# Optimization experiments

Hardware: AMD Instinct MI355X
Metric: run time of the kernel (lower is better)

## Reference

```python
import jax, jax.numpy as jnp
import numpy as np

H, W, HEADS, DIM_HEAD, SLICE = 256, 256, 8, 64, 64
SCALE = DIM_HEAD ** -0.5


def _conv(x_nhwc, w_hwio, b):
    y = jax.lax.conv_general_dilated(
        x_nhwc, w_hwio, window_strides=(1, 1), padding='SAME',
        dimension_numbers=('NHWC', 'HWIO', 'NHWC'))
    return y + b


def setup_inputs() -> dict:
    key = jax.random.key(0)
    ks = jax.random.split(key, 13)
    B, N, C, inner = 2, H * W, 128, HEADS * DIM_HEAD
    s = lambda k, shp, sc: jax.random.normal(k, shp, jnp.float32) * sc
    return {
        'x': s(ks[0], (B, N, C), 1.0),
        'Wfx': s(ks[1], (3, 3, C, inner), 0.05),
        'bfx': s(ks[2], (inner,), 0.02),
        'Wx': s(ks[3], (3, 3, C, inner), 0.05),
        'bx': s(ks[4], (inner,), 0.02),
        'Wslice': s(ks[5], (SLICE, DIM_HEAD), 0.1),
        'bslice': s(ks[6], (SLICE,), 0.02),
        'temperature': jnp.ones((1, HEADS, 1, 1), jnp.float32) * 0.5,
        'Wq': s(ks[7], (DIM_HEAD, DIM_HEAD), 0.1),
        'Wk': s(ks[8], (DIM_HEAD, DIM_HEAD), 0.1),
        'Wv': s(ks[9], (DIM_HEAD, DIM_HEAD), 0.1),
        'Wout': s(ks[10], (C, inner), 0.05),
        'bout': s(ks[11], (C,), 0.02),
    }


def reference(x, Wfx, bfx, Wx, bx, Wslice, bslice, temperature, Wq, Wk, Wv, Wout, bout):
    B, N, C = x.shape
    xg = x.reshape(B, H, W, C)                       # NHWC grid
    # conv QKV-style projections -> [B, heads, N, dim_head]
    def to_heads(y):
        return y.reshape(B, N, HEADS, DIM_HEAD).transpose(0, 2, 1, 3)
    fx_mid = to_heads(_conv(xg, Wfx, bfx))           # [B,h,N,d]
    x_mid = to_heads(_conv(xg, Wx, bx))              # [B,h,N,d]
    # slice assignment weights: softmax over slices with clamped temperature
    temp = jnp.clip(temperature, 0.1, 5.0)           # [1,h,1,1]
    logits = (jnp.einsum('bhnd,gd->bhng', x_mid, Wslice) + bslice) / temp
    slice_weights = jax.nn.softmax(logits, axis=-1)  # [B,h,N,G]
    slice_norm = slice_weights.sum(axis=2)           # [B,h,G]
    slice_token = jnp.einsum('bhnc,bhng->bhgc', fx_mid, slice_weights)
    slice_token = slice_token / (slice_norm + 1e-5)[..., None]  # [B,h,G,d]
    # small attention over slice tokens
    q = jnp.einsum('bhgd,ed->bhge', slice_token, Wq)
    k = jnp.einsum('bhgd,ed->bhge', slice_token, Wk)
    v = jnp.einsum('bhgd,ed->bhge', slice_token, Wv)
    attn = jax.nn.softmax(jnp.einsum('bhge,bhfe->bhgf', q, k) * SCALE, axis=-1)
    out_slice = jnp.einsum('bhgf,bhfe->bhge', attn, v)           # [B,h,G,d]
    # scatter back to tokens
    out_x = jnp.einsum('bhgc,bhng->bhnc', out_slice, slice_weights)
    out_x = out_x.transpose(0, 2, 1, 3).reshape(B, N, HEADS * DIM_HEAD)
    return jnp.einsum('bni,oi->bno', out_x, Wout) + bout
```

## Files before the change

kernel.cpp:

```cpp
#include <hip/hip_runtime.h>


typedef _Float16 f16;
typedef _Float16 f16x8 __attribute__((ext_vector_type(8)));
typedef _Float16 f16x4 __attribute__((ext_vector_type(4)));
typedef float    f32x4 __attribute__((ext_vector_type(4)));

static const size_t OFF_PADX = 0;
static const size_t OFF_WCAT = 17040384;
static const size_t OFF_ST   = 19399680;
static const size_t OFF_NORM = 19530752;
static const size_t OFF_OS   = 19532800;
static const size_t OFF_PT   = 19663872;
static const size_t OFF_XMID = 19794944;
static const size_t OFF_FXT  = 86903808;

__device__ __forceinline__ void ldsdma16(f16* lds, const f16* g) {
  __builtin_amdgcn_global_load_lds((__attribute__((address_space(1))) void*)g,
                                   (__attribute__((address_space(3))) void*)lds,
                                   16, 0, 0);
}

__global__ __launch_bounds__(256) void pad_kernel(const float* __restrict__ xb,
                                                  f16* __restrict__ padx) {
  int idx = blockIdx.x * 256 + threadIdx.x;
  if (idx >= 258 * 258 * 16) return;
  int c8 = (idx & 15) * 8;
  int r  = idx >> 4;
  int jp = r % 258;
  int ip = r / 258;
  f16x8 v;
  if (ip == 0 || ip == 257 || jp == 0 || jp == 257) {
#pragma unroll
    for (int j = 0; j < 8; ++j) v[j] = (f16)0.0f;
  } else {
    const float* src = xb + ((size_t)(ip - 1) * 256 + (jp - 1)) * 128 + c8;
#pragma unroll
    for (int j = 0; j < 8; ++j) v[j] = (f16)src[j];
  }
  *(f16x8*)(padx + (size_t)r * 128 + c8) = v;
}

__global__ __launch_bounds__(256) void prepw_kernel(const float* __restrict__ Wfx,
                                                    const float* __restrict__ Wx,
                                                    f16* __restrict__ wcat) {
  int idx = blockIdx.x * 256 + threadIdx.x;
  if (idx >= 9 * 1024 * 128) return;
  int ci = idx & 127;
  int t  = idx >> 7;
  int co = t & 1023;
  int tap = t >> 10;
  float v = (co < 512) ? Wfx[(size_t)(tap * 128 + ci) * 512 + co]
                       : Wx[(size_t)(tap * 128 + ci) * 512 + (co - 512)];
  wcat[idx] = (f16)v;
}

__global__ __launch_bounds__(256, 2) void conv_kernel(const f16* __restrict__ padx,
                                                      const f16* __restrict__ wcat,
                                                      const float* __restrict__ bfx,
                                                      const float* __restrict__ bx,
                                                      f16* __restrict__ xmid,
                                                      f16* __restrict__ fxT) {
  __shared__ f16 smem[33024];
  f16* As0 = smem;
  f16* As1 = smem + 8320;
  f16* Bs0 = smem + 16640;
  f16* Bs1 = smem + 24832;
  int tid = threadIdx.x;
  int wg = (blockIdx.x & 7) * 512 + (blockIdx.x >> 3);
  int nt = wg & 7;
  int mt = wg >> 3;
  int i  = mt >> 1;
  int j0 = (mt & 1) * 128;
  int n0 = nt * 128;
  int lane = tid & 63, wave = tid >> 6;
  int ln15 = lane & 15, quad = lane >> 4;
  int wm = wave & 1, wn = wave >> 1;

  f32x4 acc[4][4] = {};

  auto stageA = [&](int di, int kc, f16* dst) {
#pragma unroll
    for (int ph = 0; ph < 5; ++ph) {
      int s = ph * 256 + tid;
      if (ph < 4 || s < 1040) {
        int rr = s >> 3;
        int qq = ((s & 7) ^ (rr & 7)) * 8;
        ldsdma16(&dst[(ph * 256 + wave * 64) * 8],
                 padx + ((size_t)(i + di) * 258 + j0 + rr) * 128 + kc + qq);
      }
    }
  };
  auto stageB = [&](int tap, int kc, f16* dst) {
#pragma unroll
    for (int ph = 0; ph < 4; ++ph) {
      int s = ph * 256 + tid;
      int rr = s >> 3;
      int qq = ((s & 7) ^ (rr & 7)) * 8;
      ldsdma16(&dst[(ph * 256 + wave * 64) * 8],
               wcat + ((size_t)(tap * 1024 + n0 + rr)) * 128 + kc + qq);
    }
  };
  auto computePhase = [&](int dj, const f16* A, const f16* B) {
#pragma unroll
    for (int ks = 0; ks < 2; ++ks) {
      int q = ks * 4 + quad;
      f16x8 af[4], bfr[4];
#pragma unroll
      for (int xx = 0; xx < 4; ++xx) {
        int t  = dj + wm * 64 + xx * 16 + ln15;
        int rb = wn * 64 + xx * 16 + ln15;
        af[xx]  = *(const f16x8*)(&A[t * 64 + ((q ^ (t & 7)) * 8)]);
        bfr[xx] = *(const f16x8*)(&B[rb * 64 + ((q ^ (rb & 7)) * 8)]);
      }
      __builtin_amdgcn_s_setprio(1);
#pragma unroll
      for (int mf = 0; mf < 4; ++mf)
#pragma unroll
        for (int nf = 0; nf < 4; ++nf)
          acc[mf][nf] = __builtin_amdgcn_mfma_f32_16x16x32_f16(af[mf], bfr[nf],
                                                               acc[mf][nf], 0, 0, 0);
      __builtin_amdgcn_s_setprio(0);
    }
  };

  stageA(0, 0, As0);
  stageB(0, 0, Bs0);
  __syncthreads();

#pragma unroll
  for (int p = 0; p < 18; ++p) {
    int dj   = p % 3;
    int dikc = p / 3;
    if (p + 1 < 18) {
      int np = p + 1;
      int ndj = np % 3, ndikc = np / 3;
      int ndi = ndikc >> 1, nkc = (ndikc & 1) * 64;
      stageB(ndi * 3 + ndj, nkc, (np & 1) ? Bs1 : Bs0);
      if (ndj == 0) stageA(ndi, nkc, (ndikc & 1) ? As1 : As0);
    }
    computePhase(dj, (dikc & 1) ? As1 : As0, (p & 1) ? Bs1 : Bs0);
    __syncthreads();
  }

  size_t token0 = (size_t)i * 256 + j0;
  if (nt < 4) {
    f16* tile = smem;
#pragma unroll
    for (int nf = 0; nf < 4; ++nf) {
      int colLoc = wn * 64 + nf * 16 + ln15;
      float bias = bfx[n0 + colLoc];
#pragma unroll
      for (int mf = 0; mf < 4; ++mf) {
        int tokBase = wm * 64 + mf * 16 + quad * 4;
        f16x4 pk;
#pragma unroll
        for (int v = 0; v < 4; ++v) pk[v] = (f16)(acc[mf][nf][v] + bias);
        *(f16x4*)(&tile[colLoc * 136 + tokBase]) = pk;
      }
    }
    __syncthreads();
#pragma unroll
    for (int it2 = 0; it2 < 8; ++it2) {
      int s = it2 * 256 + tid;
      int c = s >> 4, t8 = s & 15;
      f16x8 vv = *(const f16x8*)(&tile[c * 136 + t8 * 8]);
      *(f16x8*)(fxT + (size_t)(n0 + c) * 65536 + token0 + t8 * 8) = vv;
    }
  } else {
#pragma unroll
    for (int nf = 0; nf < 4; ++nf) {
      int col = n0 + wn * 64 + nf * 16 + ln15;
      float bias = bx[col - 512];
#pragma unroll
      for (int mf = 0; mf < 4; ++mf) {
        int rbase = wm * 64 + mf * 16 + quad * 4;
#pragma unroll
        for (int v = 0; v < 4; ++v)
          xmid[(size_t)(token0 + rbase + v) * 512 + (col - 512)] =
              (f16)(acc[mf][nf][v] + bias);
      }
    }
  }
}

#define WS_S 72
#define WT_S 264
__global__ __launch_bounds__(256, 2) void slice_kernel(f16* __restrict__ xmid,
                                                       const f16* __restrict__ fxT,
                                                       const float* __restrict__ Wslice,
                                                       const float* __restrict__ bslice,
                                                       const float* __restrict__ temperature,
                                                       float* __restrict__ ST,
                                                       float* __restrict__ snorm) {
  __shared__ f16 Ws[64 * WS_S];
  __shared__ f16 Wt[64 * WT_S];
  __shared__ float red[64 * 65];
  __shared__ float redn[64];
  int tid = threadIdx.x;
  int h = blockIdx.x >> 6;
  int chunk = blockIdx.x & 63;
  int tok0 = chunk * 1024;
  int lane = tid & 63, wave = tid >> 6;
  int ln15 = lane & 15, quad = lane >> 4;

  for (int s = tid; s < 4096; s += 256)
    Ws[(s >> 6) * WS_S + (s & 63)] = (f16)Wslice[s];
  if (tid < 64) redn[tid] = 0.f;
  float tc = temperature[h];
  tc = fminf(fmaxf(tc, 0.1f), 5.0f);
  float invt = 1.0f / tc;
  float bsv[4];
#pragma unroll
  for (int nf = 0; nf < 4; ++nf) bsv[nf] = bslice[nf * 16 + ln15];
  __syncthreads();

  f32x4 acc2[4][4] = {};
  float naccv[4] = {};

  for (int it = 0; it < 4; ++it) {
    int tsub = it * 256 + wave * 64;
    f32x4 accA[4][4] = {};
#pragma unroll
    for (int kq = 0; kq < 2; ++kq) {
      f16x8 bf[4];
#pragma unroll
      for (int nf = 0; nf < 4; ++nf)
        bf[nf] = *(const f16x8*)(&Ws[(nf * 16 + ln15) * WS_S + kq * 32 + quad * 8]);
#pragma unroll
      for (int mf = 0; mf < 4; ++mf) {
        f16x8 af = *(const f16x8*)(xmid + (size_t)(tok0 + tsub + mf * 16 + ln15) * 512 +
                                   h * 64 + kq * 32 + quad * 8);
#pragma unroll
        for (int nf = 0; nf < 4; ++nf)
          accA[mf][nf] = __builtin_amdgcn_mfma_f32_16x16x32_f16(af, bf[nf], accA[mf][nf],
                                                                0, 0, 0);
      }
    }
#pragma unroll
    for (int mf = 0; mf < 4; ++mf) {
#pragma unroll
      for (int v = 0; v < 4; ++v) {
        float l[4];
#pragma unroll
        for (int nf = 0; nf < 4; ++nf) l[nf] = (accA[mf][nf][v] + bsv[nf]) * invt;
        float lm = fmaxf(fmaxf(l[0], l[1]), fmaxf(l[2], l[3]));
#pragma unroll
        for (int off = 1; off < 16; off <<= 1) lm = fmaxf(lm, __shfl_xor(lm, off, 64));
        float e[4], ssum = 0.f;
#pragma unroll
        for (int nf = 0; nf < 4; ++nf) { e[nf] = __expf(l[nf] - lm); ssum += e[nf]; }
#pragma unroll
        for (int off = 1; off < 16; off <<= 1) ssum += __shfl_xor(ssum, off, 64);
        float winv = 1.0f / ssum;
        int t_loc = tsub + mf * 16 + quad * 4 + v;
        int t_str = wave * 64 + mf * 16 + quad * 4 + v;
        f16* wrow = xmid + (size_t)(tok0 + t_loc) * 512 + h * 64;
#pragma unroll
        for (int nf = 0; nf < 4; ++nf) {
          float w = e[nf] * winv;
          naccv[nf] += w;
          f16 wh = (f16)w;
          wrow[nf * 16 + ln15] = wh;
          Wt[(nf * 16 + ln15) * WT_S + t_str] = wh;
        }
      }
    }
#pragma unroll
    for (int kq = 0; kq < 2; ++kq) {
      int kof = wave * 64 + kq * 32 + quad * 8;
      f16x8 bfB[4];
#pragma unroll
      for (int nf = 0; nf < 4; ++nf)
        bfB[nf] = *(const f16x8*)(fxT + (size_t)(h * 64 + nf * 16 + ln15) * 65536 +
                                  tok0 + it * 256 + kof);
#pragma unroll
      for (int mf = 0; mf < 4; ++mf) {
        f16x8 afB = *(const f16x8*)(&Wt[(mf * 16 + ln15) * WT_S + kof]);
#pragma unroll
        for (int nf = 0; nf < 4; ++nf)
          acc2[mf][nf] = __builtin_amdgcn_mfma_f32_16x16x32_f16(afB, bfB[nf],
                                                                acc2[mf][nf], 0, 0, 0);
      }
    }
  }

#pragma unroll
  for (int nf = 0; nf < 4; ++nf) atomicAdd(&redn[nf * 16 + ln15], naccv[nf]);

  for (int s = 0; s < 4; ++s) {
    if (wave == s) {
#pragma unroll
      for (int mf = 0; mf < 4; ++mf)
#pragma unroll
        for (int nf = 0; nf < 4; ++nf)
#pragma unroll
          for (int v = 0; v < 4; ++v) {
            int g = mf * 16 + quad * 4 + v;
            int d = nf * 16 + ln15;
            if (s == 0) red[g * 65 + d] = acc2[mf][nf][v];
            else        red[g * 65 + d] += acc2[mf][nf][v];
          }
    }
    __syncthreads();
  }
  float* stp = ST + (size_t)h * 4096;
  for (int s2 = tid; s2 < 4096; s2 += 256)
    atomicAdd(&stp[s2], red[(s2 >> 6) * 65 + (s2 & 63)]);
  if (tid < 64) atomicAdd(&snorm[h * 64 + tid], redn[tid]);
}

__global__ __launch_bounds__(256) void attn_pt_kernel(const float* __restrict__ ST,
                                                      const float* __restrict__ snorm,
                                                      const float* __restrict__ Wq,
                                                      const float* __restrict__ Wk,
                                                      const float* __restrict__ Wv,
                                                      const float* __restrict__ Wout,
                                                      f16* __restrict__ PT) {
  int h = blockIdx.x;
  __shared__ float tok[64 * 65];
  __shared__ float qs[64 * 65];
  __shared__ float ksm[64 * 65];
  __shared__ f16 vsm[64 * 65];
  int tid = threadIdx.x;
  const float* stp = ST + (size_t)h * 4096;
  const float* snp = snorm + (size_t)h * 64;
  for (int s = tid; s < 4096; s += 256) {
    int g = s >> 6, d = s & 63;
    tok[g * 65 + d] = stp[s] / (snp[g] + 1e-5f);
  }
  __syncthreads();
  int g = tid >> 2, p16 = (tid & 3) * 16;
  for (int e0 = 0; e0 < 16; ++e0) {
    int e = p16 + e0;
    const float* wq = Wq + e * 64;
    const float* wk = Wk + e * 64;
    const float* wv = Wv + e * 64;
    float aq = 0, ak = 0, av = 0;
#pragma unroll 8
    for (int d = 0; d < 64; ++d) {
      float tv = tok[g * 65 + d];
      aq += tv * wq[d];
      ak += tv * wk[d];
      av += tv * wv[d];
    }
    qs[g * 65 + e] = aq;
    ksm[g * 65 + e] = ak;
    vsm[g * 65 + e] = (f16)av;
  }
  __syncthreads();
  float* sc = tok;
  for (int f0 = 0; f0 < 16; ++f0) {
    int f = p16 + f0;
    float s = 0;
#pragma unroll 8
    for (int e = 0; e < 64; ++e) s += qs[g * 65 + e] * ksm[f * 65 + e];
    sc[g * 65 + f] = s * 0.125f;
  }
  __syncthreads();
  if (tid < 64) {
    float m = -1e30f;
    for (int f = 0; f < 64; ++f) m = fmaxf(m, sc[tid * 65 + f]);
    float ssum = 0;
    for (int f = 0; f < 64; ++f) {
      float e = __expf(sc[tid * 65 + f] - m);
      sc[tid * 65 + f] = e;
      ssum += e;
    }
    float inv = 1.0f / ssum;
    for (int f = 0; f < 64; ++f) sc[tid * 65 + f] *= inv;
  }
  __syncthreads();
  float* os = ksm;
  for (int e0 = 0; e0 < 16; ++e0) {
    int e = p16 + e0;
    float o = 0;
#pragma unroll 8
    for (int f = 0; f < 64; ++f) o += sc[g * 65 + f] * (float)vsm[f * 65 + e];
    os[g * 65 + e] = o;
  }
  __syncthreads();
  int o = tid >> 1, gh = (tid & 1) * 32;
  const float* wr = Wout + (size_t)o * 512 + h * 64;
  float wreg[64];
#pragma unroll
  for (int d = 0; d < 64; ++d) wreg[d] = wr[d];
  for (int gg = 0; gg < 32; ++gg) {
    int gI = gh + gg;
    float s = 0;
#pragma unroll
    for (int d = 0; d < 64; ++d) s += os[gI * 65 + d] * wreg[d];
    PT[(size_t)o * 512 + h * 64 + gI] = (f16)s;
  }
}

__global__ __launch_bounds__(256, 2) void final_kernel(const f16* __restrict__ xmid,
                                                       const f16* __restrict__ PT,
                                                       const float* __restrict__ bout,
                                                       float* __restrict__ outb) {
  __shared__ f16 As[128 * 64];
  __shared__ f16 Bs[128 * 64];
  int tid = threadIdx.x;
  int tok0 = blockIdx.x << 7;
  int lane = tid & 63, wave = tid >> 6;
  int ln15 = lane & 15, quad = lane >> 4;
  int wm = wave & 1, wn = wave >> 1;
  int rr[4], qq8[4];
#pragma unroll
  for (int ph = 0; ph < 4; ++ph) {
    int s = ph * 256 + tid;
    rr[ph] = s >> 3;
    qq8[ph] = ((s & 7) ^ (rr[ph] & 7)) * 8;
  }
  int wbase = wave * 512;
  f32x4 acc[4][4] = {};
  const f16* aB = xmid + (size_t)tok0 * 512;
  const f16* bB = PT;
  for (int kc = 0; kc < 512; kc += 64) {
#pragma unroll
    for (int ph = 0; ph < 4; ++ph) {
      ldsdma16(&As[ph * 2048 + wbase], aB + (size_t)rr[ph] * 512 + kc + qq8[ph]);
      ldsdma16(&Bs[ph * 2048 + wbase], bB + (size_t)rr[ph] * 512 + kc + qq8[ph]);
    }
    __syncthreads();
#pragma unroll
    for (int ks = 0; ks < 2; ++ks) {
      f16x8 af[4], bfr[4];
      int q = ks * 4 + quad;
#pragma unroll
      for (int xx = 0; xx < 4; ++xx) {
        int ra = wm * 64 + xx * 16 + ln15;
        int rb = wn * 64 + xx * 16 + ln15;
        af[xx]  = *(const f16x8*)(&As[ra * 64 + (q ^ (ra & 7)) * 8]);
        bfr[xx] = *(const f16x8*)(&Bs[rb * 64 + (q ^ (rb & 7)) * 8]);
      }
#pragma unroll
      for (int mf = 0; mf < 4; ++mf)
#pragma unroll
        for (int nf = 0; nf < 4; ++nf)
          acc[mf][nf] = __builtin_amdgcn_mfma_f32_16x16x32_f16(af[mf], bfr[nf],
                                                               acc[mf][nf], 0, 0, 0);
    }
    __syncthreads();
  }
#pragma unroll
  for (int nf = 0; nf < 4; ++nf) {
    int col = wn * 64 + nf * 16 + ln15;
    float bo = bout[col];
#pragma unroll
    for (int mf = 0; mf < 4; ++mf) {
      int rbase = wm * 64 + mf * 16 + quad * 4;
#pragma unroll
      for (int v = 0; v < 4; ++v)
        outb[(size_t)(tok0 + rbase + v) * 128 + col] = acc[mf][nf][v] + bo;
    }
  }
}

extern "C" void kernel_launch(void* const* d_in, const int* in_sizes, int n_in,
                              void* d_out, int out_size, void* d_ws, size_t ws_size,
                              hipStream_t stream) {
  const float* x    = (const float*)d_in[0];
  const float* Wfx  = (const float*)d_in[1];
  const float* bfx  = (const float*)d_in[2];
  const float* Wx   = (const float*)d_in[3];
  const float* bx   = (const float*)d_in[4];
  const float* Wsl  = (const float*)d_in[5];
  const float* bsl  = (const float*)d_in[6];
  const float* temp = (const float*)d_in[7];
  const float* Wq   = (const float*)d_in[8];
  const float* Wk   = (const float*)d_in[9];
  const float* Wv   = (const float*)d_in[10];
  const float* Wout = (const float*)d_in[11];
  const float* bout = (const float*)d_in[12];
  float* out = (float*)d_out;
  char* ws = (char*)d_ws;

  f16*  padx = (f16*)(ws + OFF_PADX);
  f16*  wcat = (f16*)(ws + OFF_WCAT);
  float* ST  = (float*)(ws + OFF_ST);
  float* nrm = (float*)(ws + OFF_NORM);
  f16*  PT   = (f16*)(ws + OFF_PT);
  f16*  xmid = (f16*)(ws + OFF_XMID);
  f16*  fxT  = (f16*)(ws + OFF_FXT);

  prepw_kernel<<<4608, 256, 0, stream>>>(Wfx, Wx, wcat);
  for (int b = 0; b < 2; ++b) {
    const float* xb = x + (size_t)b * 65536 * 128;
    float* outb = out + (size_t)b * 65536 * 128;
    (void)hipMemsetAsync(ws + OFF_ST, 0, 131072 + 2048, stream);
    pad_kernel<<<4161, 256, 0, stream>>>(xb, padx);
    conv_kernel<<<4096, 256, 0, stream>>>(padx, wcat, bfx, bx, xmid, fxT);
    slice_kernel<<<512, 256, 0, stream>>>(xmid, fxT, Wsl, bsl, temp, ST, nrm);
    attn_pt_kernel<<<8, 256, 0, stream>>>(ST, nrm, Wq, Wk, Wv, Wout, PT);
    final_kernel<<<512, 256, 0, stream>>>(xmid, PT, bout, outb);
  }
}
```

Measured before the change: 829.1 us.

## Single-buffer A tile, triple-buffer B with depth-2 prefetch and fine vmcnt waits

Restructures the conv GEMM main loop so B (weight) tiles are triple-buffered and prefetched two phases ahead, while A uses a single buffer. For the third horizontal tap, A fragments are copied into registers early so the next A tile can be loaded into the same LDS buffer. Full __syncthreads is replaced by partial s_waitcnt vmcnt waits plus raw barriers, so outstanding DMA loads can overlap compute. The risk is synchronization correctness around the reused A buffer and higher register pressure from the preloaded fragments.

Result: no change. 823.8 us (-0.6%).

```diff
diff --git a/kernel.cpp b/kernel.cpp
--- a/kernel.cpp
+++ b/kernel.cpp
@@ -10,7 +10,6 @@
 static const size_t OFF_WCAT = 17040384;
 static const size_t OFF_ST   = 19399680;
 static const size_t OFF_NORM = 19530752;
-static const size_t OFF_OS   = 19532800;
 static const size_t OFF_PT   = 19663872;
 static const size_t OFF_XMID = 19794944;
 static const size_t OFF_FXT  = 86903808;
@@ -19,6 +18,16 @@
   __builtin_amdgcn_global_load_lds((__attribute__((address_space(1))) void*)g,
                                    (__attribute__((address_space(3))) void*)lds,
                                    16, 0, 0);
+}
+
+template <int N>
+__device__ __forceinline__ void vmwait() {
+  asm volatile("s_waitcnt vmcnt(%0)" ::"n"(N) : "memory");
+}
+__device__ __forceinline__ void phase_barrier() {
+  __builtin_amdgcn_s_barrier();
+  __builtin_amdgcn_sched_barrier(0);
+  asm volatile("" ::: "memory");
 }
 
 __global__ __launch_bounds__(256) void pad_kernel(const float* __restrict__ xb,
@@ -61,11 +70,11 @@
                                                       const float* __restrict__ bx,
                                                       f16* __restrict__ xmid,
                                                       f16* __restrict__ fxT) {
-  __shared__ f16 smem[33024];
-  f16* As0 = smem;
-  f16* As1 = smem + 8320;
-  f16* Bs0 = smem + 16640;
-  f16* Bs1 = smem + 24832;
+  __shared__ f16 smem[34816];
+  f16* As  = smem;
+  f16* Bs0 = smem + 10240;
+  f16* Bs1 = smem + 18432;
+  f16* Bs2 = smem + 26624;
   int tid = threadIdx.x;
   int wg = (blockIdx.x & 7) * 512 + (blockIdx.x >> 3);
   int nt = wg & 7;
@@ -79,16 +88,15 @@
 
   f32x4 acc[4][4] = {};
 
-  auto stageA = [&](int di, int kc, f16* dst) {
+  auto stageA = [&](int di, int kc) {
 #pragma unroll
     for (int ph = 0; ph < 5; ++ph) {
       int s = ph * 256 + tid;
-      if (ph < 4 || s < 1040) {
-        int rr = s >> 3;
-        int qq = ((s & 7) ^ (rr & 7)) * 8;
-        ldsdma16(&dst[(ph * 256 + wave * 64) * 8],
-                 padx + ((size_t)(i + di) * 258 + j0 + rr) * 128 + kc + qq);
-      }
+      int rr = s >> 3;
+      int rrc = rr < 130 ? rr : 129;
+      int qq = ((s & 7) ^ (rr & 7)) * 8;
+      ldsdma16(&As[(ph * 256 + wave * 64) * 8],
+               padx + ((size_t)(i + di) * 258 + j0 + rrc) * 128 + kc + qq);
     }
   };
   auto stageB = [&](int tap, int kc, f16* dst) {
@@ -101,7 +109,7 @@
                wcat + ((size_t)(tap * 1024 + n0 + rr)) * 128 + kc + qq);
     }
   };
-  auto computePhase = [&](int dj, const f16* A, const f16* B) {
+  auto computeA = [&](int dj, const f16* B) {
 #pragma unroll
     for (int ks = 0; ks < 2; ++ks) {
       int q = ks * 4 + quad;
@@ -110,7 +118,7 @@
       for (int xx = 0; xx < 4; ++xx) {
         int t  = dj + wm * 64 + xx * 16 + ln15;
         int rb = wn * 64 + xx * 16 + ln15;
-        af[xx]  = *(const f16x8*)(&A[t * 64 + ((q ^ (t & 7)) * 8)]);
+        af[xx]  = *(const f16x8*)(&As[t * 64 + ((q ^ (t & 7)) * 8)]);
         bfr[xx] = *(const f16x8*)(&B[rb * 64 + ((q ^ (rb & 7)) * 8)]);
       }
       __builtin_amdgcn_s_setprio(1);
@@ -124,23 +132,68 @@
     }
   };
 
-  stageA(0, 0, As0);
+  f16x8 afr[2][4];
+  auto preloadAfr = [&]() {
+#pragma unroll
+    for (int ks = 0; ks < 2; ++ks) {
+      int q = ks * 4 + quad;
+#pragma unroll
+      for (int xx = 0; xx < 4; ++xx) {
+        int t = 2 + wm * 64 + xx * 16 + ln15;
+        afr[ks][xx] = *(const f16x8*)(&As[t * 64 + ((q ^ (t & 7)) * 8)]);
+      }
+    }
+  };
+  auto computeR = [&](const f16* B) {
+#pragma unroll
+    for (int ks = 0; ks < 2; ++ks) {
+      int q = ks * 4 + quad;
+      f16x8 bfr[4];
+#pragma unroll
+      for (int xx = 0; xx < 4; ++xx) {
+        int rb = wn * 64 + xx * 16 + ln15;
+        bfr[xx] = *(const f16x8*)(&B[rb * 64 + ((q ^ (rb & 7)) * 8)]);
+      }
+      __builtin_amdgcn_s_setprio(1);
+#pragma unroll
+      for (int mf = 0; mf < 4; ++mf)
+#pragma unroll
+        for (int nf = 0; nf < 4; ++nf)
+          acc[mf][nf] = __builtin_amdgcn_mfma_f32_16x16x32_f16(afr[ks][mf], bfr[nf],
+                                                               acc[mf][nf], 0, 0, 0);
+      __builtin_amdgcn_s_setprio(0);
+    }
+  };
+
+  stageA(0, 0);
   stageB(0, 0, Bs0);
-  __syncthreads();
+  stageB(1, 0, Bs1);
+  vmwait<4>();
+  phase_barrier();
 
 #pragma unroll
   for (int p = 0; p < 18; ++p) {
-    int dj   = p % 3;
-    int dikc = p / 3;
-    if (p + 1 < 18) {
-      int np = p + 1;
-      int ndj = np % 3, ndikc = np / 3;
-      int ndi = ndikc >> 1, nkc = (ndikc & 1) * 64;
-      stageB(ndi * 3 + ndj, nkc, (np & 1) ? Bs1 : Bs0);
-      if (ndj == 0) stageA(ndi, nkc, (ndikc & 1) ? As1 : As0);
-    }
-    computePhase(dj, (dikc & 1) ? As1 : As0, (p & 1) ? Bs1 : Bs0);
-    __syncthreads();
+    int dj = p % 3;
+    int d  = p / 3;
+    if (dj == 2 && d < 5) {
+      int dg = d + 1;
+      stageA(dg >> 1, (dg & 1) * 64);
+    }
+    if (p + 2 < 18) {
+      int np = p + 2;
+      int ndikc = np / 3;
+      int ntap = (ndikc >> 1) * 3 + (np % 3);
+      int nkc  = (ndikc & 1) * 64;
+      f16* dst = (np % 3 == 0) ? Bs0 : (np % 3 == 1) ? Bs1 : Bs2;
+      stageB(ntap, nkc, dst);
+    }
+    const f16* Bp = (p % 3 == 0) ? Bs0 : (p % 3 == 1) ? Bs1 : Bs2;
+    if (dj == 1) preloadAfr();
+    if (dj < 2) computeA(dj, Bp);
+    else        computeR(Bp);
+    if (p < 16)      vmwait<4>();
+    else if (p == 16) vmwait<0>();
+    if (p < 17) phase_barrier();
   }
 
   size_t token0 = (size_t)i * 256 + j0;
```

## Pre-swizzle conv weights into MFMA fragment order and read B directly from global

Applied to the files above, without the earlier changes.

The weight-prep kernel now writes the conv weights already laid out in per-lane MFMA B-fragment order. The conv kernel drops B staging through LDS and loads B fragments straight from global/L2 with coalesced 16-byte loads. This halves LDS use so launch bounds go to 4 blocks per CU, and it restructures the main loop so A is staged once per (di, kc) and reused across three dj taps. The cost is that every wave issues global B loads inside the compute loop with no prefetch, so L2 latency can be exposed and B traffic is duplicated across waves (wm).

After: 916.3 us. +10.5%, slower.

```diff
diff --git a/kernel.cpp b/kernel.cpp
--- a/kernel.cpp
+++ b/kernel.cpp
@@ -7,10 +7,9 @@
 typedef float    f32x4 __attribute__((ext_vector_type(4)));
 
 static const size_t OFF_PADX = 0;
-static const size_t OFF_WCAT = 17040384;
+static const size_t OFF_BFRG = 17040384;
 static const size_t OFF_ST   = 19399680;
 static const size_t OFF_NORM = 19530752;
-static const size_t OFF_OS   = 19532800;
 static const size_t OFF_PT   = 19663872;
 static const size_t OFF_XMID = 19794944;
 static const size_t OFF_FXT  = 86903808;
@@ -43,29 +42,33 @@
 
 __global__ __launch_bounds__(256) void prepw_kernel(const float* __restrict__ Wfx,
                                                     const float* __restrict__ Wx,
-                                                    f16* __restrict__ wcat) {
+                                                    f16* __restrict__ bf) {
   int idx = blockIdx.x * 256 + threadIdx.x;
-  if (idx >= 9 * 1024 * 128) return;
-  int ci = idx & 127;
-  int t  = idx >> 7;
-  int co = t & 1023;
-  int tap = t >> 10;
+  if (idx >= 1179648) return;
+  int e    = idx & 7;
+  int lane = (idx >> 3) & 63;
+  int xx   = (idx >> 9) & 3;
+  int ks   = (idx >> 11) & 1;
+  int wn   = (idx >> 12) & 1;
+  int nt   = (idx >> 13) & 7;
+  int kc2  = (idx >> 16) & 1;
+  int tap  = idx >> 17;
+  int co = nt * 128 + wn * 64 + xx * 16 + (lane & 15);
+  int ci = kc2 * 64 + (ks * 4 + (lane >> 4)) * 8 + e;
   float v = (co < 512) ? Wfx[(size_t)(tap * 128 + ci) * 512 + co]
                        : Wx[(size_t)(tap * 128 + ci) * 512 + (co - 512)];
-  wcat[idx] = (f16)v;
-}
-
-__global__ __launch_bounds__(256, 2) void conv_kernel(const f16* __restrict__ padx,
-                                                      const f16* __restrict__ wcat,
+  bf[idx] = (f16)v;
+}
+
+__global__ __launch_bounds__(256, 4) void conv_kernel(const f16* __restrict__ padx,
+                                                      const f16* __restrict__ Bfrag,
                                                       const float* __restrict__ bfx,
                                                       const float* __restrict__ bx,
                                                       f16* __restrict__ xmid,
                                                       f16* __restrict__ fxT) {
-  __shared__ f16 smem[33024];
+  __shared__ f16 smem[17408];
   f16* As0 = smem;
   f16* As1 = smem + 8320;
-  f16* Bs0 = smem + 16640;
-  f16* Bs1 = smem + 24832;
   int tid = threadIdx.x;
   int wg = (blockIdx.x & 7) * 512 + (blockIdx.x >> 3);
   int nt = wg & 7;
@@ -91,27 +94,16 @@
       }
     }
   };
-  auto stageB = [&](int tap, int kc, f16* dst) {
-#pragma unroll
-    for (int ph = 0; ph < 4; ++ph) {
-      int s = ph * 256 + tid;
-      int rr = s >> 3;
-      int qq = ((s & 7) ^ (rr & 7)) * 8;
-      ldsdma16(&dst[(ph * 256 + wave * 64) * 8],
-               wcat + ((size_t)(tap * 1024 + n0 + rr)) * 128 + kc + qq);
-    }
-  };
-  auto computePhase = [&](int dj, const f16* A, const f16* B) {
+  auto computePhase = [&](int dj, const f16* A, const f16* Bw) {
 #pragma unroll
     for (int ks = 0; ks < 2; ++ks) {
       int q = ks * 4 + quad;
       f16x8 af[4], bfr[4];
 #pragma unroll
       for (int xx = 0; xx < 4; ++xx) {
-        int t  = dj + wm * 64 + xx * 16 + ln15;
-        int rb = wn * 64 + xx * 16 + ln15;
+        int t = dj + wm * 64 + xx * 16 + ln15;
         af[xx]  = *(const f16x8*)(&A[t * 64 + ((q ^ (t & 7)) * 8)]);
-        bfr[xx] = *(const f16x8*)(&B[rb * 64 + ((q ^ (rb & 7)) * 8)]);
+        bfr[xx] = *(const f16x8*)(Bw + (ks * 4 + xx) * 512 + lane * 8);
       }
       __builtin_amdgcn_s_setprio(1);
 #pragma unroll
@@ -125,21 +117,19 @@
   };
 
   stageA(0, 0, As0);
-  stageB(0, 0, Bs0);
-  __syncthreads();
-
-#pragma unroll
-  for (int p = 0; p < 18; ++p) {
-    int dj   = p % 3;
-    int dikc = p / 3;
-    if (p + 1 < 18) {
-      int np = p + 1;
-      int ndj = np % 3, ndikc = np / 3;
-      int ndi = ndikc >> 1, nkc = (ndikc & 1) * 64;
-      stageB(ndi * 3 + ndj, nkc, (np & 1) ? Bs1 : Bs0);
-      if (ndj == 0) stageA(ndi, nkc, (ndikc & 1) ? As1 : As0);
-    }
-    computePhase(dj, (dikc & 1) ? As1 : As0, (p & 1) ? Bs1 : Bs0);
+  __syncthreads();
+
+#pragma unroll
+  for (int d = 0; d < 6; ++d) {
+    int di = d >> 1, kc2 = d & 1;
+    if (d + 1 < 6) stageA((d + 1) >> 1, ((d + 1) & 1) * 64, (d & 1) ? As0 : As1);
+    const f16* A = (d & 1) ? As1 : As0;
+#pragma unroll
+    for (int dj = 0; dj < 3; ++dj) {
+      int tap = di * 3 + dj;
+      const f16* Bw = Bfrag + ((size_t)(((tap * 2 + kc2) * 8 + nt) * 2 + wn)) * 4096;
+      computePhase(dj, A, Bw);
+    }
     __syncthreads();
   }
 
@@ -477,20 +467,20 @@
   char* ws = (char*)d_ws;
 
   f16*  padx = (f16*)(ws + OFF_PADX);
-  f16*  wcat = (f16*)(ws + OFF_WCAT);
+  f16*  Bfrg = (f16*)(ws + OFF_BFRG);
   float* ST  = (float*)(ws + OFF_ST);
   float* nrm = (float*)(ws + OFF_NORM);
   f16*  PT   = (f16*)(ws + OFF_PT);
   f16*  xmid = (f16*)(ws + OFF_XMID);
   f16*  fxT  = (f16*)(ws + OFF_FXT);
 
-  prepw_kernel<<<4608, 256, 0, stream>>>(Wfx, Wx, wcat);
+  prepw_kernel<<<4608, 256, 0, stream>>>(Wfx, Wx, Bfrg);
   for (int b = 0; b < 2; ++b) {
     const float* xb = x + (size_t)b * 65536 * 128;
     float* outb = out + (size_t)b * 65536 * 128;
     (void)hipMemsetAsync(ws + OFF_ST, 0, 131072 + 2048, stream);
     pad_kernel<<<4161, 256, 0, stream>>>(xb, padx);
-    conv_kernel<<<4096, 256, 0, stream>>>(padx, wcat, bfx, bx, xmid, fxT);
+    conv_kernel<<<4096, 256, 0, stream>>>(padx, Bfrg, bfx, bx, xmid, fxT);
     slice_kernel<<<512, 256, 0, stream>>>(xmid, fxT, Wsl, bsl, temp, ST, nrm);
     attn_pt_kernel<<<8, 256, 0, stream>>>(ST, nrm, Wq, Wk, Wv, Wout, PT);
     final_kernel<<<512, 256, 0, stream>>>(xmid, PT, bout, outb);
```
